# Optimization experiments

Measured on AMD Instinct MI355X. Metric: run time of the kernel, lower is better.

Reference implementation:

```python
import jax, jax.numpy as jnp
import numpy as np

B, N, C, OUT, E = 8, 16384, 128, 256, 262144


def setup_inputs() -> dict:
    key = jax.random.key(0)
    k1, k2, k3 = jax.random.split(key, 3)
    x = jax.random.normal(k1, (B, N, C), dtype=jnp.float32)
    edge_index = jax.random.randint(k2, (2, E), 0, N, dtype=jnp.int64)
    W = jax.random.normal(k3, (C, OUT), dtype=jnp.float32) * 0.02
    b = jnp.zeros((OUT,), dtype=jnp.float32)
    return {"x": x, "edge_index": edge_index, "W": W, "b": b}


def reference(x, edge_index, W, b):
    # x: (B, N, C); edge_index: (2, E) shared across the batch (as in the torch code,
    # which repeats row/col B times with batch offsets -> equivalent to per-batch segment max).
    row, col = edge_index[0], edge_index[1]
    n = x.shape[1]

    def agg_one(xb):  # xb: (N, C)
        x_j = xb[col]  # gather neighbor features, (E, C)
        a = jax.ops.segment_max(x_j, row, num_segments=n)  # amax scatter-reduce
        # nodes with no incoming edge: torch fills -1e9 then zeros them; segment_max gives -inf
        return jnp.where(jnp.isfinite(a), a, 0.0)

    aggr = jax.vmap(agg_one)(x) - x  # max-relative: max_j(x_j) - x_i, (B, N, C)
    h = jnp.einsum("bnc,co->bno", aggr, W) + b
    return jax.nn.gelu(h, approximate=False)  # torch nn.GELU() is exact erf GELU
```

## Files before the change

### kernel.cpp

```cpp
#include <hip/hip_runtime.h>
#include <hip/hip_bf16.h>

#define B_   8
#define N_   16384
#define C_   128
#define OUT_ 256
#define E_   262144

#define CNT_OFF  0u
#define OVFC_OFF 16384u
#define OVF_OFF  16448u
#define TAB_OFF  540736u
#define WT_OFF   1589312u
#define XBF_OFF  1605696u
#define AGGR_OFF 9994304u

typedef __attribute__((ext_vector_type(8))) short bf16x8;
typedef __attribute__((ext_vector_type(4))) float f32x4;

__device__ __forceinline__ unsigned short f2bf(float f) {
  unsigned u = __float_as_uint(f);
  u += 0x7FFFu + ((u >> 16) & 1u);
  return (unsigned short)(u >> 16);
}
__device__ __forceinline__ float gelu_exact(float v) {
  return 0.5f * v * (1.0f + erff(v * 0.70710678118654752f));
}

__global__ __launch_bounds__(256) void k_prep(const float* __restrict__ x,
                                              const unsigned* __restrict__ eidx,
                                              const float* __restrict__ W,
                                              unsigned* __restrict__ ws) {
  const unsigned bid = blockIdx.x, tid = threadIdx.x;
  if (bid < 16384u) {
    unsigned i = bid * 256u + tid;
    float4 v = ((const float4*)x)[i];
    uint2 o;
    o.x = (unsigned)f2bf(v.x) | ((unsigned)f2bf(v.y) << 16);
    o.y = (unsigned)f2bf(v.z) | ((unsigned)f2bf(v.w) << 16);
    ((uint2*)(ws + XBF_OFF))[i] = o;
  } else if (bid < 17408u) {
    __shared__ int flag32;
    if (tid == 0) flag32 = 0;
    __syncthreads();
    unsigned e = (bid - 16384u) * 256u + tid;
    if (eidx[2u * e + 1u] != 0u) flag32 = 1;
    __syncthreads();
    int row, col;
    if (flag32) {
      row = (int)eidx[e];
      col = (int)eidx[e + E_];
    } else {
      const long long* p = (const long long*)eidx;
      row = (int)p[e];
      col = (int)p[e + E_];
    }
    unsigned pos = atomicAdd(ws + CNT_OFF + (unsigned)row, 1u);
    if (pos < 64u) {
      ws[TAB_OFF + ((unsigned)row << 6) + pos] = (unsigned)col;
    } else {
      unsigned o = atomicAdd(ws + OVFC_OFF, 1u);
      ws[OVF_OFF + 2u * o]      = (unsigned)row;
      ws[OVF_OFF + 2u * o + 1u] = (unsigned)col;
    }
  } else {
    unsigned t = (bid - 17408u) * 256u + tid;
    unsigned n = t >> 7, k = t & 127u;
    ((unsigned short*)(ws + WT_OFF))[n * 128u + k] = f2bf(W[k * 256u + n]);
  }
}

__global__ __launch_bounds__(256) void k_aggr(const uint4* __restrict__ xbf4,
                                              const unsigned* __restrict__ ws,
                                              uint4* __restrict__ aggr4) {
  const unsigned bi = blockIdx.x;
  const unsigned b  = bi & 7u;
  const unsigned rg = bi >> 3;
  const unsigned row = (rg << 2) | (threadIdx.x >> 6);
  const unsigned lane = threadIdx.x & 63u;
  const unsigned g  = lane >> 4;
  const unsigned ln = lane & 15u;
  const unsigned* tab = ws + TAB_OFF;
  const uint4* xb = xbf4 + ((size_t)b << 18);

  const unsigned deg = ws[CNT_OFF + row];
  const bool has = (deg != 0u);
  const unsigned d64 = deg < 64u ? deg : 64u;

  const unsigned cpre = tab[(row << 6) + lane];

  float mlo[4], mhi[4];
#pragma unroll
  for (int r = 0; r < 4; ++r) { mlo[r] = -INFINITY; mhi[r] = -INFINITY; }

#define MAX1(a, r)                                                          \
  mhi[r] = fmaxf(mhi[r], __uint_as_float(a));                               \
  mlo[r] = fmaxf(mlo[r], __uint_as_float((a) << 16));
#define MAX2(a, c, r)                                                       \
  mhi[r] = fmaxf(mhi[r], fmaxf(__uint_as_float(a), __uint_as_float(c)));    \
  mlo[r] = fmaxf(mlo[r],                                                    \
      fmaxf(__uint_as_float((a) << 16), __uint_as_float((c) << 16)));

  unsigned t = 0u;
  while (t + 16u <= d64) {
    unsigned c0 = (unsigned)__shfl((int)cpre, (int)(t + g));
    unsigned c1 = (unsigned)__shfl((int)cpre, (int)(t + 4u + g));
    unsigned c2 = (unsigned)__shfl((int)cpre, (int)(t + 8u + g));
    unsigned c3 = (unsigned)__shfl((int)cpre, (int)(t + 12u + g));
    uint4 u0 = xb[((size_t)c0 << 4) + ln];
    uint4 u1 = xb[((size_t)c1 << 4) + ln];
    uint4 u2 = xb[((size_t)c2 << 4) + ln];
    uint4 u3 = xb[((size_t)c3 << 4) + ln];
    MAX2(u0.x, u1.x, 0) MAX2(u0.y, u1.y, 1)
    MAX2(u0.z, u1.z, 2) MAX2(u0.w, u1.w, 3)
    MAX2(u2.x, u3.x, 0) MAX2(u2.y, u3.y, 1)
    MAX2(u2.z, u3.z, 2) MAX2(u2.w, u3.w, 3)
    t += 16u;
  }
  if (t + 8u <= d64) {
    unsigned c0 = (unsigned)__shfl((int)cpre, (int)(t + g));
    unsigned c1 = (unsigned)__shfl((int)cpre, (int)(t + 4u + g));
    uint4 u0 = xb[((size_t)c0 << 4) + ln];
    uint4 u1 = xb[((size_t)c1 << 4) + ln];
    MAX2(u0.x, u1.x, 0) MAX2(u0.y, u1.y, 1)
    MAX2(u0.z, u1.z, 2) MAX2(u0.w, u1.w, 3)
    t += 8u;
  }
  if (t + 4u <= d64) {
    unsigned c = (unsigned)__shfl((int)cpre, (int)(t + g));
    uint4 u = xb[((size_t)c << 4) + ln];
    MAX1(u.x, 0) MAX1(u.y, 1) MAX1(u.z, 2) MAX1(u.w, 3)
    t += 4u;
  }
  {
    unsigned rem = d64 - t;
    unsigned c = (unsigned)__shfl((int)cpre, (int)((t + g) & 63u));
    if (g < rem) {
      uint4 u = xb[((size_t)c << 4) + ln];
      MAX1(u.x, 0) MAX1(u.y, 1) MAX1(u.z, 2) MAX1(u.w, 3)
    }
  }
  if (deg > 64u) {
    unsigned no = ws[OVFC_OFF];
    for (unsigned i = 0u; i < no; i += 4u) {
      unsigned k = i + g;
      if (k < no && ws[OVF_OFF + 2u * k] == row) {
        unsigned c = ws[OVF_OFF + 2u * k + 1u];
        uint4 u = xb[((size_t)c << 4) + ln];
        MAX1(u.x, 0) MAX1(u.y, 1) MAX1(u.z, 2) MAX1(u.w, 3)
      }
    }
  }
#undef MAX1
#undef MAX2

#pragma unroll
  for (int r = 0; r < 4; ++r) {
    mlo[r] = fmaxf(mlo[r], __shfl_xor(mlo[r], 16, 64));
    mhi[r] = fmaxf(mhi[r], __shfl_xor(mhi[r], 16, 64));
  }
#pragma unroll
  for (int r = 0; r < 4; ++r) {
    mlo[r] = fmaxf(mlo[r], __shfl_xor(mlo[r], 32, 64));
    mhi[r] = fmaxf(mhi[r], __shfl_xor(mhi[r], 32, 64));
  }

  if (g == 0u) {
    const uint4 xw = xb[((size_t)row << 4) + ln];
    unsigned xv[4] = {xw.x, xw.y, xw.z, xw.w};
    unsigned ox[4];
#pragma unroll
    for (int r = 0; r < 4; ++r) {
      float vlo = has ? mlo[r] : 0.0f;
      float vhi = has ? __uint_as_float(__float_as_uint(mhi[r]) & 0xFFFF0000u)
                      : 0.0f;
      unsigned lo = f2bf(vlo - __uint_as_float(xv[r] << 16));
      unsigned hi = f2bf(vhi - __uint_as_float(xv[r] & 0xFFFF0000u));
      ox[r] = lo | (hi << 16);
    }
    uint4 o = {ox[0], ox[1], ox[2], ox[3]};
    aggr4[(((size_t)b << 14) + row) * 16u + ln] = o;
  }
}

__global__ __launch_bounds__(256, 4) void k_gemm(const unsigned short* __restrict__ aggr,
                                                 const unsigned short* __restrict__ Wt,
                                                 const float* __restrict__ bias,
                                                 float* __restrict__ out) {
  __shared__ unsigned short Wt_sm[128 * 136];
  const int tid = threadIdx.x;
  const int nbase = blockIdx.x * 128;
  const int mbase = blockIdx.y * 64;

#pragma unroll
  for (int i = 0; i < 8; ++i) {
    int slot = i * 256 + tid;
    int n = slot >> 4, k8 = slot & 15;
    uint4 u = *(const uint4*)(Wt + (size_t)(nbase + n) * 128 + k8 * 8);
    *(uint4*)&Wt_sm[n * 136 + k8 * 8] = u;
  }
  __syncthreads();

  const int lane = tid & 63;
  const int wv = tid >> 6;
  const int ln = lane & 15;
  const int q = lane >> 4;

  const unsigned short* arow = aggr + (size_t)(mbase + wv * 16 + ln) * 128 + q * 8;
  bf16x8 af[4];
#pragma unroll
  for (int kc = 0; kc < 4; ++kc) af[kc] = *(const bf16x8*)(arow + kc * 32);

  f32x4 acc[8];
#pragma unroll
  for (int f = 0; f < 8; ++f) acc[f] = (f32x4){0.f, 0.f, 0.f, 0.f};

#pragma unroll
  for (int kc = 0; kc < 4; ++kc) {
#pragma unroll
    for (int f = 0; f < 8; ++f) {
      bf16x8 bf = *(const bf16x8*)&Wt_sm[(f * 16 + ln) * 136 + kc * 32 + q * 8];
      acc[f] = __builtin_amdgcn_mfma_f32_16x16x32_bf16(af[kc], bf, acc[f], 0, 0, 0);
    }
  }

#pragma unroll
  for (int f = 0; f < 8; ++f) {
    int n = nbase + f * 16 + ln;
    float bv = bias[n];
#pragma unroll
    for (int r = 0; r < 4; ++r) {
      int m = mbase + wv * 16 + q * 4 + r;
      out[(size_t)m * 256 + n] = gelu_exact(acc[f][r] + bv);
    }
  }
}

extern "C" void kernel_launch(void* const* d_in, const int* in_sizes, int n_in,
                              void* d_out, int out_size, void* d_ws, size_t ws_size,
                              hipStream_t stream) {
  const float* x      = (const float*)d_in[0];
  const unsigned* eid = (const unsigned*)d_in[1];
  const float* W      = (const float*)d_in[2];
  const float* bia    = (const float*)d_in[3];
  float* out          = (float*)d_out;
  unsigned* ws        = (unsigned*)d_ws;

  unsigned short* Wt   = (unsigned short*)(ws + WT_OFF);
  unsigned short* aggr = (unsigned short*)(ws + AGGR_OFF);

  hipMemsetAsync(ws + CNT_OFF, 0, 16448 * sizeof(unsigned), stream);
  hipLaunchKernelGGL(k_prep, dim3(17536),   dim3(256), 0, stream, x, eid, W, ws);
  hipLaunchKernelGGL(k_aggr, dim3(32768),   dim3(256), 0, stream,
                     (const uint4*)(ws + XBF_OFF), ws, (uint4*)(ws + AGGR_OFF));
  hipLaunchKernelGGL(k_gemm, dim3(2, 2048), dim3(256), 0, stream,
                     aggr, Wt, bia, out);
}
```

Measured before the change: 284.5 us.

## Branch-free padded gather by degree class, hoist self load, full-N GEMM blocks

The aggregation kernel replaces the cascading 16/8/4/remainder loops with degree-class branches. These issue fixed batches of gathers whose indices are clamped to the last valid neighbor, which is safe for max. This trades some redundant loads for more memory-level parallelism and fewer branches. The self-row load is hoisted to the start so it overlaps the gathers. The GEMM now has each block cover all 256 output columns in two halves, so the A fragment is loaded once and reused, at the cost of reloading W into shared memory twice and adding extra barriers.

Result: no change. 289.4 us (+1.7%).

```diff
diff --git a/kernel.cpp b/kernel.cpp
--- a/kernel.cpp
+++ b/kernel.cpp
@@ -25,6 +25,9 @@
 }
 __device__ __forceinline__ float gelu_exact(float v) {
   return 0.5f * v * (1.0f + erff(v * 0.70710678118654752f));
+}
+__device__ __forceinline__ unsigned umin_(unsigned a, unsigned b) {
+  return a < b ? a : b;
 }
 
 __global__ __launch_bounds__(256) void k_prep(const float* __restrict__ x,
@@ -80,14 +83,14 @@
   const unsigned lane = threadIdx.x & 63u;
   const unsigned g  = lane >> 4;
   const unsigned ln = lane & 15u;
-  const unsigned* tab = ws + TAB_OFF;
   const uint4* xb = xbf4 + ((size_t)b << 18);
 
   const unsigned deg = ws[CNT_OFF + row];
   const bool has = (deg != 0u);
   const unsigned d64 = deg < 64u ? deg : 64u;
 
-  const unsigned cpre = tab[(row << 6) + lane];
+  const unsigned cpre = ws[TAB_OFF + (row << 6) + lane];
+  const uint4 xw = xb[((size_t)row << 4) + ln];
 
   float mlo[4], mhi[4];
 #pragma unroll
@@ -101,43 +104,49 @@
   mlo[r] = fmaxf(mlo[r],                                                    \
       fmaxf(__uint_as_float((a) << 16), __uint_as_float((c) << 16)));
 
-  unsigned t = 0u;
-  while (t + 16u <= d64) {
-    unsigned c0 = (unsigned)__shfl((int)cpre, (int)(t + g));
-    unsigned c1 = (unsigned)__shfl((int)cpre, (int)(t + 4u + g));
-    unsigned c2 = (unsigned)__shfl((int)cpre, (int)(t + 8u + g));
-    unsigned c3 = (unsigned)__shfl((int)cpre, (int)(t + 12u + g));
-    uint4 u0 = xb[((size_t)c0 << 4) + ln];
-    uint4 u1 = xb[((size_t)c1 << 4) + ln];
-    uint4 u2 = xb[((size_t)c2 << 4) + ln];
-    uint4 u3 = xb[((size_t)c3 << 4) + ln];
-    MAX2(u0.x, u1.x, 0) MAX2(u0.y, u1.y, 1)
-    MAX2(u0.z, u1.z, 2) MAX2(u0.w, u1.w, 3)
-    MAX2(u2.x, u3.x, 0) MAX2(u2.y, u3.y, 1)
-    MAX2(u2.z, u3.z, 2) MAX2(u2.w, u3.w, 3)
-    t += 16u;
-  }
-  if (t + 8u <= d64) {
-    unsigned c0 = (unsigned)__shfl((int)cpre, (int)(t + g));
-    unsigned c1 = (unsigned)__shfl((int)cpre, (int)(t + 4u + g));
-    uint4 u0 = xb[((size_t)c0 << 4) + ln];
-    uint4 u1 = xb[((size_t)c1 << 4) + ln];
-    MAX2(u0.x, u1.x, 0) MAX2(u0.y, u1.y, 1)
-    MAX2(u0.z, u1.z, 2) MAX2(u0.w, u1.w, 3)
-    t += 8u;
-  }
-  if (t + 4u <= d64) {
-    unsigned c = (unsigned)__shfl((int)cpre, (int)(t + g));
-    uint4 u = xb[((size_t)c << 4) + ln];
-    MAX1(u.x, 0) MAX1(u.y, 1) MAX1(u.z, 2) MAX1(u.w, 3)
-    t += 4u;
-  }
-  {
-    unsigned rem = d64 - t;
-    unsigned c = (unsigned)__shfl((int)cpre, (int)((t + g) & 63u));
-    if (g < rem) {
-      uint4 u = xb[((size_t)c << 4) + ln];
-      MAX1(u.x, 0) MAX1(u.y, 1) MAX1(u.z, 2) MAX1(u.w, 3)
+  if (has) {
+    const unsigned dm1 = d64 - 1u;
+    if (d64 <= 16u) {
+      unsigned c0 = (unsigned)__shfl((int)cpre, (int)umin_(g,       dm1));
+      unsigned c1 = (unsigned)__shfl((int)cpre, (int)umin_(4u + g,  dm1));
+      unsigned c2 = (unsigned)__shfl((int)cpre, (int)umin_(8u + g,  dm1));
+      unsigned c3 = (unsigned)__shfl((int)cpre, (int)umin_(12u + g, dm1));
+      uint4 u0 = xb[((size_t)c0 << 4) + ln];
+      uint4 u1 = xb[((size_t)c1 << 4) + ln];
+      uint4 u2 = xb[((size_t)c2 << 4) + ln];
+      uint4 u3 = xb[((size_t)c3 << 4) + ln];
+      MAX2(u0.x, u1.x, 0) MAX2(u0.y, u1.y, 1)
+      MAX2(u0.z, u1.z, 2) MAX2(u0.w, u1.w, 3)
+      MAX2(u2.x, u3.x, 0) MAX2(u2.y, u3.y, 1)
+      MAX2(u2.z, u3.z, 2) MAX2(u2.w, u3.w, 3)
+    } else if (d64 <= 32u) {
+      unsigned c[8];
+#pragma unroll
+      for (int i = 0; i < 8; ++i)
+        c[i] = (unsigned)__shfl((int)cpre, (int)umin_(4u * i + g, dm1));
+      uint4 u[8];
+#pragma unroll
+      for (int i = 0; i < 8; ++i) u[i] = xb[((size_t)c[i] << 4) + ln];
+#pragma unroll
+      for (int i = 0; i < 8; i += 2) {
+        MAX2(u[i].x, u[i + 1].x, 0) MAX2(u[i].y, u[i + 1].y, 1)
+        MAX2(u[i].z, u[i + 1].z, 2) MAX2(u[i].w, u[i + 1].w, 3)
+      }
+    } else {
+      for (unsigned t = 0u; t < d64; t += 16u) {
+        unsigned c0 = (unsigned)__shfl((int)cpre, (int)umin_(t + g,       dm1));
+        unsigned c1 = (unsigned)__shfl((int)cpre, (int)umin_(t + 4u + g,  dm1));
+        unsigned c2 = (unsigned)__shfl((int)cpre, (int)umin_(t + 8u + g,  dm1));
+        unsigned c3 = (unsigned)__shfl((int)cpre, (int)umin_(t + 12u + g, dm1));
+        uint4 u0 = xb[((size_t)c0 << 4) + ln];
+        uint4 u1 = xb[((size_t)c1 << 4) + ln];
+        uint4 u2 = xb[((size_t)c2 << 4) + ln];
+        uint4 u3 = xb[((size_t)c3 << 4) + ln];
+        MAX2(u0.x, u1.x, 0) MAX2(u0.y, u1.y, 1)
+        MAX2(u0.z, u1.z, 2) MAX2(u0.w, u1.w, 3)
+        MAX2(u2.x, u3.x, 0) MAX2(u2.y, u3.y, 1)
+        MAX2(u2.z, u3.z, 2) MAX2(u2.w, u3.w, 3)
+      }
     }
   }
   if (deg > 64u) {
@@ -166,7 +175,6 @@
   }
 
   if (g == 0u) {
-    const uint4 xw = xb[((size_t)row << 4) + ln];
     unsigned xv[4] = {xw.x, xw.y, xw.z, xw.w};
     unsigned ox[4];
 #pragma unroll
@@ -189,17 +197,7 @@
                                                  float* __restrict__ out) {
   __shared__ unsigned short Wt_sm[128 * 136];
   const int tid = threadIdx.x;
-  const int nbase = blockIdx.x * 128;
-  const int mbase = blockIdx.y * 64;
-
-#pragma unroll
-  for (int i = 0; i < 8; ++i) {
-    int slot = i * 256 + tid;
-    int n = slot >> 4, k8 = slot & 15;
-    uint4 u = *(const uint4*)(Wt + (size_t)(nbase + n) * 128 + k8 * 8);
-    *(uint4*)&Wt_sm[n * 136 + k8 * 8] = u;
-  }
-  __syncthreads();
+  const int mbase = blockIdx.x * 64;
 
   const int lane = tid & 63;
   const int wv = tid >> 6;
@@ -211,28 +209,42 @@
 #pragma unroll
   for (int kc = 0; kc < 4; ++kc) af[kc] = *(const bf16x8*)(arow + kc * 32);
 
-  f32x4 acc[8];
-#pragma unroll
-  for (int f = 0; f < 8; ++f) acc[f] = (f32x4){0.f, 0.f, 0.f, 0.f};
-
-#pragma unroll
-  for (int kc = 0; kc < 4; ++kc) {
+#pragma unroll
+  for (int half = 0; half < 2; ++half) {
+    const int nbase = half * 128;
+#pragma unroll
+    for (int i = 0; i < 8; ++i) {
+      int slot = i * 256 + tid;
+      int n = slot >> 4, k8 = slot & 15;
+      uint4 u = *(const uint4*)(Wt + (size_t)(nbase + n) * 128 + k8 * 8);
+      *(uint4*)&Wt_sm[n * 136 + k8 * 8] = u;
+    }
+    __syncthreads();
+
+    f32x4 acc[8];
+#pragma unroll
+    for (int f = 0; f < 8; ++f) acc[f] = (f32x4){0.f, 0.f, 0.f, 0.f};
+
+#pragma unroll
+    for (int kc = 0; kc < 4; ++kc) {
+#pragma unroll
+      for (int f = 0; f < 8; ++f) {
+        bf16x8 bf = *(const bf16x8*)&Wt_sm[(f * 16 + ln) * 136 + kc * 32 + q * 8];
+        acc[f] = __builtin_amdgcn_mfma_f32_16x16x32_bf16(af[kc], bf, acc[f], 0, 0, 0);
+      }
+    }
+
 #pragma unroll
     for (int f = 0; f < 8; ++f) {
-      bf16x8 bf = *(const bf16x8*)&Wt_sm[(f * 16 + ln) * 136 + kc * 32 + q * 8];
-      acc[f] = __builtin_amdgcn_mfma_f32_16x16x32_bf16(af[kc], bf, acc[f], 0, 0, 0);
-    }
-  }
-
-#pragma unroll
-  for (int f = 0; f < 8; ++f) {
-    int n = nbase + f * 16 + ln;
-    float bv = bias[n];
-#pragma unroll
-    for (int r = 0; r < 4; ++r) {
-      int m = mbase + wv * 16 + q * 4 + r;
-      out[(size_t)m * 256 + n] = gelu_exact(acc[f][r] + bv);
-    }
+      int n = nbase + f * 16 + ln;
+      float bv = bias[n];
+#pragma unroll
+      for (int r = 0; r < 4; ++r) {
+        int m = mbase + wv * 16 + q * 4 + r;
+        out[(size_t)m * 256 + n] = gelu_exact(acc[f][r] + bv);
+      }
+    }
+    __syncthreads();
   }
 }
 
@@ -250,9 +262,9 @@
   unsigned short* aggr = (unsigned short*)(ws + AGGR_OFF);
 
   hipMemsetAsync(ws + CNT_OFF, 0, 16448 * sizeof(unsigned), stream);
-  hipLaunchKernelGGL(k_prep, dim3(17536),   dim3(256), 0, stream, x, eid, W, ws);
-  hipLaunchKernelGGL(k_aggr, dim3(32768),   dim3(256), 0, stream,
+  hipLaunchKernelGGL(k_prep, dim3(17536), dim3(256), 0, stream, x, eid, W, ws);
+  hipLaunchKernelGGL(k_aggr, dim3(32768), dim3(256), 0, stream,
                      (const uint4*)(ws + XBF_OFF), ws, (uint4*)(ws + AGGR_OFF));
-  hipLaunchKernelGGL(k_gemm, dim3(2, 2048), dim3(256), 0, stream,
+  hipLaunchKernelGGL(k_gemm, dim3(2048),  dim3(256), 0, stream,
                      aggr, Wt, bia, out);
 }
```
